# Kernel optimization log

Hardware: AMD Instinct MI355X
Metric: run time of the kernel (lower is better)

Reference implementation:

```python
import jax, jax.numpy as jnp
import numpy as np

B, T, D = 4, 2048, 1024
NF = 512
NB = 4
FREQ_SCALE = 0.1


def _w(k, shape, scale):
    return jax.random.normal(k, shape, jnp.float32) * scale


def setup_inputs() -> dict:
    key = jax.random.key(0)
    ks = jax.random.split(key, 16)
    d = D ** -0.5
    inp = {}
    inp['x'] = jax.random.normal(ks[0], (B, T, D), jnp.float32)
    inp['norm_g'] = jnp.ones((D,), jnp.float32)
    inp['norm_b'] = jnp.zeros((D,), jnp.float32)
    inp['Wconcept'] = _w(ks[1], (D, D), d); inp['bconcept'] = jnp.zeros((D,), jnp.float32)
    inp['Wcg'] = _w(ks[2], (D, D), d); inp['bcg'] = jnp.zeros((D,), jnp.float32)
    inp['Wfg'] = _w(ks[3], (NF, D), d); inp['bfg'] = jnp.zeros((NF,), jnp.float32)
    inp['Wtg'] = _w(ks[4], (1, D), d); inp['btg'] = jnp.zeros((1,), jnp.float32)
    inp['Wband'] = _w(ks[5], (NB, D), d); inp['bband'] = jnp.zeros((NB,), jnp.float32)
    inp['Wsp'] = _w(ks[6], (2 * NF, D), d)  # to_spectral, no bias
    inp['freq_importance'] = jnp.ones((NF,), jnp.float32)
    inp['log_decay'] = (jnp.linspace(-3.0, -0.001, NF) + _w(ks[7], (NF,), 0.1)).astype(jnp.float32)
    inp['frequencies'] = ((jnp.arange(NF, dtype=jnp.float32) / NF * 2.0 - 1.0) * 0.2)
    inp['dt'] = jnp.ones((NF,), jnp.float32) * 0.5
    inp['Wgate'] = _w(ks[8], (D, D), d); inp['bgate'] = jnp.zeros((D,), jnp.float32)
    inp['Wfs'] = _w(ks[9], (D, 2 * NF), (2 * NF) ** -0.5)  # from_spectral, no bias
    inp['output_scale'] = jnp.ones((1,), jnp.float32) * 0.5
    inp['norm2_g'] = jnp.ones((D,), jnp.float32)
    inp['norm2_b'] = jnp.zeros((D,), jnp.float32)
    inp['W1'] = _w(ks[10], (4 * D, D), d); inp['b1'] = jnp.zeros((4 * D,), jnp.float32)
    inp['W2'] = _w(ks[11], (D, 4 * D), (4 * D) ** -0.5); inp['b2'] = jnp.zeros((D,), jnp.float32)
    return inp


def _ln(x, g, b):
    m = jnp.mean(x, axis=-1, keepdims=True)
    v = jnp.var(x, axis=-1, keepdims=True)
    return (x - m) * jax.lax.rsqrt(v + 1e-5) * g + b


def reference(x, norm_g, norm_b, Wconcept, bconcept, Wcg, bcg, Wfg, bfg, Wtg, btg,
              Wband, bband, Wsp, freq_importance, log_decay, frequencies, dt,
              Wgate, bgate, Wfs, output_scale, norm2_g, norm2_b, W1, b1, W2, b2):
    b_, t_, _ = x.shape
    nf = log_decay.shape[0]
    nb = Wband.shape[0]
    residual = x
    xn = _ln(x, norm_g, norm_b)

    concept = xn @ Wconcept.T + bconcept
    concept_preserved = concept * jax.nn.sigmoid(xn @ Wcg.T + bcg)

    forget_gates = jax.nn.sigmoid(xn @ Wfg.T + bfg)          # (B,T,NF)
    temporal_strength = jax.nn.sigmoid(xn @ Wtg.T + btg)     # (B,T,1)
    band_strengths = jax.nn.sigmoid(xn @ Wband.T + bband)    # (B,T,NB)

    sp = xn @ Wsp.T                                          # (B,T,2*NF)
    u = jax.lax.complex(sp[..., :nf], sp[..., nf:]) * forget_gates

    decay = jax.nn.sigmoid(log_decay) * (jax.nn.softmax(freq_importance) * nf)
    omega = frequencies * FREQ_SCALE * (jax.nn.sigmoid(dt) * 2.0)
    rot = jax.lax.complex(jnp.cos(omega), jnp.sin(omega))    # (NF,)
    A = decay * rot                                          # (NF,) complex

    band_scale = jnp.repeat(band_strengths, nf // nb, axis=-1)  # (B,T,NF)
    A_exp = A * band_scale                                   # (B,T,NF) complex

    ones_first = jnp.ones((b_, 1, nf), A_exp.dtype)
    powers = jnp.cumprod(jnp.concatenate([ones_first, A_exp[:, :-1, :]], axis=1), axis=1)
    powers = powers * temporal_strength
    kernel = powers * rot

    n_fft = 2 * t_
    Uf = jnp.fft.fft(u, n=n_fft, axis=1)
    Kf = jnp.fft.fft(kernel, n=n_fft, axis=1)
    y = jnp.fft.ifft(Uf * Kf, n=n_fft, axis=1)[:, :t_, :]

    spectral_out = jnp.concatenate([y.real, y.imag], axis=-1)
    y_proj = (spectral_out @ Wfs.T) * output_scale
    gate_values = jax.nn.sigmoid(xn @ Wgate.T + bgate)
    y_gated = (y_proj * gate_values + concept_preserved) / 2.0  # dropout: eval mode

    x2 = residual + y_gated
    xn2 = _ln(x2, norm2_g, norm2_b)
    h = jax.nn.gelu(xn2 @ W1.T + b1, approximate=False)
    return x2 + h @ W2.T + b2
```

## Files before the change

### kernel.cpp

```cpp
#include <hip/hip_runtime.h>
#include <hip/hip_bf16.h>
#include <cstdint>
#include <cstddef>

typedef unsigned short u16;
typedef unsigned int u32;
typedef short bf16x8 __attribute__((ext_vector_type(8)));
typedef float f32x4 __attribute__((ext_vector_type(4)));
typedef float f32x2 __attribute__((ext_vector_type(2)));

static constexpr int Bb = 4, Tt = 2048, Dd = 1024, NFf = 512, NBb = 4;
static constexpr int Mm = Bb * Tt;
static constexpr int NZz = 4736;
static constexpr int Lc = 32;

#define DEV __device__ __forceinline__

typedef const __attribute__((address_space(1))) u32* gas_p;
typedef __attribute__((address_space(3))) u32* las_p;

DEV u16 f2bf(float f) {
    uint32_t u = __float_as_uint(f);
    u = (u + 0x7FFF + ((u >> 16) & 1)) >> 16;
    return (u16)u;
}
DEV float bf2f(u16 h) { return __uint_as_float(((uint32_t)h) << 16); }
DEV float sigm(float x) { return 1.0f / (1.0f + __expf(-x)); }
DEV float gelu_ex(float t) { return 0.5f * t * (1.0f + erff(t * 0.70710678118f)); }

DEV void xcd_swizzle(int& bx, int& by) {
    int gx = gridDim.x, nwg = gx * gridDim.y;
    int lin = blockIdx.x + gx * blockIdx.y;
    int q = nwg >> 3, r = nwg & 7;
    int xcd = lin & 7, idx = lin >> 3;
    int wg = (xcd < r) ? (xcd * (q + 1) + idx) : (r * (q + 1) + (xcd - r) * q + idx);
    bx = wg % gx; by = wg / gx;
}

static constexpr int NW0 = NZz * Dd;
static constexpr int NW1 = Dd * 2 * NFf;
static constexpr int NW2 = 4 * Dd * Dd;
static constexpr int NW3 = 4 * Dd * Dd;
static constexpr int NWTOT = NW0 + NW1 + NW2 + NW3;
static constexpr int NWB4 = NWTOT / 1024;

__global__ __launch_bounds__(256) void prep_all(
    const float* __restrict__ Wconcept, const float* __restrict__ Wcg,
    const float* __restrict__ Wfg, const float* __restrict__ Wgate,
    const float* __restrict__ Wsp, const float* __restrict__ Wtg,
    const float* __restrict__ Wband,
    const float* __restrict__ bconcept, const float* __restrict__ bcg,
    const float* __restrict__ bfg, const float* __restrict__ bgate,
    const float* __restrict__ btg, const float* __restrict__ bband,
    const float* __restrict__ Wfs, const float* __restrict__ W1,
    const float* __restrict__ W2,
    const float* __restrict__ fi, const float* __restrict__ logd,
    const float* __restrict__ freqs, const float* __restrict__ dtv,
    const float* __restrict__ x, const float* __restrict__ norm_g,
    const float* __restrict__ norm_b,
    u16* __restrict__ wcat, float* __restrict__ bias_cat,
    u16* __restrict__ wfs, u16* __restrict__ w1b, u16* __restrict__ w2b,
    float* __restrict__ rr, float* __restrict__ ri,
    float* __restrict__ Ar, float* __restrict__ Ai,
    u16* __restrict__ xn)
{
    const int bx = blockIdx.x;
    if (bx == 0) {
        __shared__ float red[256];
        int t = threadIdx.x;
        float v0 = fi[t], v1 = fi[t + 256];
        red[t] = fmaxf(v0, v1); __syncthreads();
        for (int s = 128; s; s >>= 1) { if (t < s) red[t] = fmaxf(red[t], red[t + s]); __syncthreads(); }
        float mx = red[0]; __syncthreads();
        float e0 = expf(v0 - mx), e1 = expf(v1 - mx);
        red[t] = e0 + e1; __syncthreads();
        for (int s = 128; s; s >>= 1) { if (t < s) red[t] += red[t + s]; __syncthreads(); }
        float inv = 1.0f / red[0];
#pragma unroll
        for (int k = 0; k < 2; k++) {
            int f = t + k * 256;
            float e = k ? e1 : e0;
            float decay = sigm(logd[f]) * (e * inv * (float)NFf);
            float omega = freqs[f] * 0.1f * (sigm(dtv[f]) * 2.0f);
            float cc = cosf(omega), ss = sinf(omega);
            rr[f] = cc; ri[f] = ss; Ar[f] = decay * cc; Ai[f] = decay * ss;
        }
        return;
    }
    if (bx <= NWB4) {
        const int i = ((bx - 1) * 256 + threadIdx.x) * 4;
        if (i < NW0) {
            int r = i >> 10, c = i & 1023;
            float4 v = {0.f, 0.f, 0.f, 0.f};
            if      (r < 1024) v = *(const float4*)(Wconcept + r * 1024 + c);
            else if (r < 2048) v = *(const float4*)(Wcg + (r - 1024) * 1024 + c);
            else if (r < 2560) v = *(const float4*)(Wfg + (r - 2048) * 1024 + c);
            else if (r < 3584) v = *(const float4*)(Wgate + (r - 2560) * 1024 + c);
            else if (r < 4608) v = *(const float4*)(Wsp + (r - 3584) * 1024 + c);
            else if (r == 4608) v = *(const float4*)(Wtg + c);
            else if (r < 4613) v = *(const float4*)(Wband + (r - 4609) * 1024 + c);
            ushort4 o{f2bf(v.x), f2bf(v.y), f2bf(v.z), f2bf(v.w)};
            *(ushort4*)(wcat + i) = o;
            if (c == 0) {
                float bv;
                if      (r < 1024) bv = bconcept[r];
                else if (r < 2048) bv = bcg[r - 1024];
                else if (r < 2560) bv = bfg[r - 2048];
                else if (r < 3584) bv = bgate[r - 2560];
                else if (r < 4608) bv = 0.0f;
                else if (r == 4608) bv = btg[0];
                else if (r < 4613) bv = bband[r - 4609];
                else bv = 0.0f;
                bias_cat[r] = bv;
            }
        } else if (i < NW0 + NW1) {
            int j = i - NW0;
            float4 v = *(const float4*)(Wfs + j);
            *(ushort4*)(wfs + j) = ushort4{f2bf(v.x), f2bf(v.y), f2bf(v.z), f2bf(v.w)};
        } else if (i < NW0 + NW1 + NW2) {
            int j = i - NW0 - NW1;
            float4 v = *(const float4*)(W1 + j);
            *(ushort4*)(w1b + j) = ushort4{f2bf(v.x), f2bf(v.y), f2bf(v.z), f2bf(v.w)};
        } else {
            int j = i - NW0 - NW1 - NW2;
            float4 v = *(const float4*)(W2 + j);
            *(ushort4*)(w2b + j) = ushort4{f2bf(v.x), f2bf(v.y), f2bf(v.z), f2bf(v.w)};
        }
        return;
    }
    const int m = bx - NWB4 - 1, tid = threadIdx.x;
    float4 v = ((const float4*)(x + (size_t)m * Dd))[tid];
    float s1 = v.x + v.y + v.z + v.w;
    float s2 = v.x * v.x + v.y * v.y + v.z * v.z + v.w * v.w;
    __shared__ float lds[16];
    for (int o = 32; o; o >>= 1) { s1 += __shfl_down(s1, o); s2 += __shfl_down(s2, o); }
    int lane = tid & 63, w = tid >> 6;
    if (!lane) { lds[w] = s1; lds[8 + w] = s2; }
    __syncthreads();
    s1 = lds[0] + lds[1] + lds[2] + lds[3];
    s2 = lds[8] + lds[9] + lds[10] + lds[11];
    float mean = s1 * (1.0f / Dd);
    float var  = s2 * (1.0f / Dd) - mean * mean;
    float rstd = rsqrtf(var + 1e-5f);
    float4 gv = ((const float4*)norm_g)[tid];
    float4 bv = ((const float4*)norm_b)[tid];
    ushort4 o;
    o.x = f2bf((v.x - mean) * rstd * gv.x + bv.x);
    o.y = f2bf((v.y - mean) * rstd * gv.y + bv.y);
    o.z = f2bf((v.z - mean) * rstd * gv.z + bv.z);
    o.w = f2bf((v.w - mean) * rstd * gv.w + bv.w);
    ((ushort4*)(xn + (size_t)m * Dd))[tid] = o;
}

template<int MODE>
__global__ __launch_bounds__(256, 3) void gemm_bt(
    const u16* __restrict__ A, const u16* __restrict__ Bw,
    const float* __restrict__ bias, const u16* __restrict__ addb,
    void* __restrict__ Cout, int M, int N, int K)
{
    __shared__ __align__(16) u16 smA[128 * 64];
    __shared__ __align__(16) u16 smB[128 * 64];
    const int tid = threadIdx.x;
    int bxs, bys;
    xcd_swizzle(bxs, bys);
    const int m0 = bxs * 128;
    const int n0 = bys * 128;
    const int w = tid >> 6, lane = tid & 63;
    const int wr = w >> 1, wc = w & 1;
    const int quad = lane >> 4, l16 = lane & 15;

    const int r0 = tid >> 3;
    const int cs = (tid & 7) ^ (r0 & 7);
    const u16* gA = A + (size_t)(m0 + r0) * K + cs * 8;
    const u16* gB = Bw + (size_t)(n0 + r0) * K + cs * 8;

    const int swzf = l16 & 7;

    f32x4 acc[4][4];
#pragma unroll
    for (int i = 0; i < 4; i++)
#pragma unroll
        for (int j = 0; j < 4; j++) acc[i][j] = {0.f, 0.f, 0.f, 0.f};

    for (int k0 = 0; k0 < K; k0 += 64) {
        __syncthreads();
#pragma unroll
        for (int j = 0; j < 4; j++) {
            __builtin_amdgcn_global_load_lds((gas_p)(gA + k0 + (size_t)(j * 32) * K),
                                             (las_p)(smA + j * 2048 + tid * 8), 16, 0, 0);
            __builtin_amdgcn_global_load_lds((gas_p)(gB + k0 + (size_t)(j * 32) * K),
                                             (las_p)(smB + j * 2048 + tid * 8), 16, 0, 0);
        }
        __syncthreads();
#pragma unroll
        for (int seg = 0; seg < 2; seg++) {
            bf16x8 af[4], bfv[4];
#pragma unroll
            for (int mi = 0; mi < 4; mi++)
                af[mi] = *(const bf16x8*)&smA[(wr * 64 + mi * 16 + l16) * 64 +
                                              (((seg * 4 + quad) ^ swzf) * 8)];
#pragma unroll
            for (int ni = 0; ni < 4; ni++)
                bfv[ni] = *(const bf16x8*)&smB[(wc * 64 + ni * 16 + l16) * 64 +
                                               (((seg * 4 + quad) ^ swzf) * 8)];
#pragma unroll
            for (int mi = 0; mi < 4; mi++)
#pragma unroll
                for (int ni = 0; ni < 4; ni++)
                    acc[mi][ni] = __builtin_amdgcn_mfma_f32_16x16x32_bf16(
                        af[mi], bfv[ni], acc[mi][ni], 0, 0, 0);
        }
    }

#pragma unroll
    for (int mi = 0; mi < 4; mi++) {
#pragma unroll
        for (int ni = 0; ni < 4; ni++) {
            const int gn = n0 + wc * 64 + ni * 16 + l16;
            const int gm0 = m0 + wr * 64 + mi * 16 + quad * 4;
            if constexpr (MODE == 0 || MODE == 2 || MODE == 4) {
                float bv = (MODE == 4) ? 0.0f : bias[gn];
                float t0 = acc[mi][ni][0] + bv, t1 = acc[mi][ni][1] + bv;
                float t2 = acc[mi][ni][2] + bv, t3 = acc[mi][ni][3] + bv;
                if constexpr (MODE == 2) {
                    t0 = gelu_ex(t0); t1 = gelu_ex(t1); t2 = gelu_ex(t2); t3 = gelu_ex(t3);
                }
                __hip_bfloat162 h01 = __float22bfloat162_rn(float2{t0, t1});
                __hip_bfloat162 h23 = __float22bfloat162_rn(float2{t2, t3});
                __hip_bfloat16* o = (__hip_bfloat16*)Cout;
                o[(size_t)(gm0 + 0) * N + gn] = h01.x;
                o[(size_t)(gm0 + 1) * N + gn] = h01.y;
                o[(size_t)(gm0 + 2) * N + gn] = h23.x;
                o[(size_t)(gm0 + 3) * N + gn] = h23.y;
            } else {
#pragma unroll
                for (int r = 0; r < 4; r++) {
                    const int gm = gm0 + r;
                    ((float*)Cout)[(size_t)gm * N + gn] =
                        acc[mi][ni][r] + bias[gn] + bf2f(addb[(size_t)gm * N + gn]);
                }
            }
        }
    }
}

__global__ __launch_bounds__(256) void prepAk_kernel(
    const u16* __restrict__ Z, ushort2* __restrict__ u2b,
    const float* __restrict__ Ar, const float* __restrict__ Ai,
    const float* __restrict__ rr, const float* __restrict__ ri,
    f32x2* __restrict__ k2)
{
    const int bx = blockIdx.x;
    if (bx < Mm) {
        const int m = bx, t = threadIdx.x;
        const u16* zr = Z + (size_t)m * NZz;
        ushort2 fgh = *(const ushort2*)(zr + 2048 + 2 * t);
        ushort2 spr = *(const ushort2*)(zr + 3584 + 2 * t);
        ushort2 spi = *(const ushort2*)(zr + 4096 + 2 * t);
        float fg0 = sigm(bf2f(fgh.x)), fg1 = sigm(bf2f(fgh.y));
        ushort4 o;
        o.x = f2bf(bf2f(spr.x) * fg0); o.y = f2bf(bf2f(spi.x) * fg0);
        o.z = f2bf(bf2f(spr.y) * fg1); o.w = f2bf(bf2f(spi.y) * fg1);
        ((ushort4*)u2b)[m * 256 + t] = o;
        return;
    }
    int g = (bx - Mm) * 256 + threadIdx.x;
    int b = g >> 9, f = g & (NFf - 1);
    float Pr = 1.0f, Pi = 0.0f;
    float ar = Ar[f], ai = Ai[f], cr = rr[f], ci = ri[f];
    const int band = f >> 7;
    const u16* zb = Z + (size_t)(b * Tt) * NZz;
    for (int tau = 0; tau < Lc; tau++) {
        const u16* zrow = zb + (size_t)tau * NZz;
        float tsv = sigm(bf2f(zrow[4608]));
        k2[((size_t)b * Lc + tau) * NFf + f] = f32x2{tsv * (cr * Pr - ci * Pi),
                                                     tsv * (cr * Pi + ci * Pr)};
        float bsv = sigm(bf2f(zrow[4609 + band]));
        float er = ar * bsv, ei = ai * bsv;
        float nPr = Pr * er - Pi * ei;
        float nPi = Pr * ei + Pi * er;
        Pr = nPr; Pi = nPi;
    }
}

__global__ __launch_bounds__(256) void conv_kernel(
    const ushort2* __restrict__ u2b, const f32x2* __restrict__ k2,
    u16* __restrict__ spec)
{
    __shared__ f32x2 su[96 * 64];
    __shared__ f32x2 sk[Lc * 64];
    const int tid = threadIdx.x;
    const int fl = tid & 63;
    const int ty = tid >> 6;
    const int f0 = blockIdx.x * 64;
    const int t0 = blockIdx.y * 64;
    const int b  = blockIdx.z;

    for (int i = tid; i < Lc * 64; i += 256) {
        int tau = i >> 6, ff = i & 63;
        sk[i] = k2[((size_t)b * Lc + tau) * NFf + f0 + ff];
    }
    for (int i = tid; i < 96 * 64; i += 256) {
        int r = i >> 6, ff = i & 63;
        int t = t0 - 32 + r;
        f32x2 v = {0.f, 0.f};
        if (t >= 0) {
            ushort2 h = u2b[((size_t)b * Tt + t) * NFf + f0 + ff];
            v = f32x2{bf2f(h.x), bf2f(h.y)};
        }
        su[i] = v;
    }
    __syncthreads();

    const int tl0 = 32 + ty * 16;
    f32x2 win[16], y[16];
#pragma unroll
    for (int j = 0; j < 16; j++) {
        win[j] = su[(tl0 + j) * 64 + fl];
        y[j] = f32x2{0.f, 0.f};
    }
#pragma unroll
    for (int tau = 0; tau < Lc; tau++) {
        f32x2 k = sk[tau * 64 + fl];
#pragma unroll
        for (int j = 0; j < 16; j++) {
            y[j].x += win[j].x * k.x - win[j].y * k.y;
            y[j].y += win[j].x * k.y + win[j].y * k.x;
        }
#pragma unroll
        for (int j = 15; j >= 1; j--) win[j] = win[j - 1];
        win[0] = su[(tl0 - tau - 1) * 64 + fl];
    }
#pragma unroll
    for (int j = 0; j < 16; j++) {
        size_t row = (size_t)(b * Tt + t0 + ty * 16 + j);
        spec[row * (2 * NFf) + f0 + fl]       = f2bf(y[j].x);
        spec[row * (2 * NFf) + NFf + f0 + fl] = f2bf(y[j].y);
    }
}

__global__ __launch_bounds__(256) void fuse2_ln_kernel(
    const float* __restrict__ x, const u16* __restrict__ Z,
    const u16* __restrict__ P2, const float* __restrict__ osc,
    const float* __restrict__ g2, const float* __restrict__ b2v,
    u16* __restrict__ x2b, u16* __restrict__ xn2)
{
    const int m = blockIdx.x, tid = threadIdx.x;
    const float os = osc[0];
    const u16* zr = Z + (size_t)m * NZz;
    float4 xv = ((const float4*)(x + (size_t)m * Dd))[tid];
    ushort4 pv = ((const ushort4*)(P2 + (size_t)m * Dd))[tid];
    ushort4 cv = *(const ushort4*)(zr + tid * 4);
    ushort4 gv = *(const ushort4*)(zr + 1024 + tid * 4);
    ushort4 av = *(const ushort4*)(zr + 2560 + tid * 4);
    float vals[4]; float s1 = 0.0f, s2 = 0.0f;
#pragma unroll
    for (int j = 0; j < 4; j++) {
        float concept = bf2f((&cv.x)[j]);
        float cg   = sigm(bf2f((&gv.x)[j]));
        float gate = sigm(bf2f((&av.x)[j]));
        float p = bf2f((&pv.x)[j]);
        float v = (&xv.x)[j] + 0.5f * (p * os * gate + concept * cg);
        vals[j] = v; s1 += v; s2 += v * v;
    }
    __shared__ float lds[16];
    for (int o = 32; o; o >>= 1) { s1 += __shfl_down(s1, o); s2 += __shfl_down(s2, o); }
    int lane = tid & 63, w = tid >> 6;
    if (!lane) { lds[w] = s1; lds[8 + w] = s2; }
    __syncthreads();
    s1 = lds[0] + lds[1] + lds[2] + lds[3];
    s2 = lds[8] + lds[9] + lds[10] + lds[11];
    float mean = s1 * (1.0f / Dd);
    float var  = s2 * (1.0f / Dd) - mean * mean;
    float rstd = rsqrtf(var + 1e-5f);
    ushort4 xo, no;
#pragma unroll
    for (int j = 0; j < 4; j++) {
        int d = tid * 4 + j;
        (&xo.x)[j] = f2bf(vals[j]);
        (&no.x)[j] = f2bf((vals[j] - mean) * rstd * g2[d] + b2v[d]);
    }
    ((ushort4*)(x2b + (size_t)m * Dd))[tid] = xo;
    ((ushort4*)(xn2 + (size_t)m * Dd))[tid] = no;
}

extern "C" void kernel_launch(void* const* d_in, const int* in_sizes, int n_in,
                              void* d_out, int out_size, void* d_ws, size_t ws_size,
                              hipStream_t stream)
{
    const float* x        = (const float*)d_in[0];
    const float* norm_g   = (const float*)d_in[1];
    const float* norm_b   = (const float*)d_in[2];
    const float* Wconcept = (const float*)d_in[3];
    const float* bconcept = (const float*)d_in[4];
    const float* Wcg      = (const float*)d_in[5];
    const float* bcg      = (const float*)d_in[6];
    const float* Wfg      = (const float*)d_in[7];
    const float* bfg      = (const float*)d_in[8];
    const float* Wtg      = (const float*)d_in[9];
    const float* btg      = (const float*)d_in[10];
    const float* Wband    = (const float*)d_in[11];
    const float* bband    = (const float*)d_in[12];
    const float* Wsp      = (const float*)d_in[13];
    const float* fi       = (const float*)d_in[14];
    const float* logd     = (const float*)d_in[15];
    const float* freqs    = (const float*)d_in[16];
    const float* dtv      = (const float*)d_in[17];
    const float* Wgate    = (const float*)d_in[18];
    const float* bgate    = (const float*)d_in[19];
    const float* Wfs      = (const float*)d_in[20];
    const float* osc      = (const float*)d_in[21];
    const float* n2g      = (const float*)d_in[22];
    const float* n2b      = (const float*)d_in[23];
    const float* W1       = (const float*)d_in[24];
    const float* b1       = (const float*)d_in[25];
    const float* W2       = (const float*)d_in[26];
    const float* b2       = (const float*)d_in[27];

    char* ws = (char*)d_ws;
    size_t off = 0;
    auto alloc = [&](size_t bytes) { size_t c = off; off += (bytes + 255) & ~(size_t)255; return c; };
    size_t o_wcat = alloc((size_t)NZz * Dd * 2);
    size_t o_bias = alloc((size_t)NZz * 4);
    size_t o_wfs  = alloc((size_t)Dd * 2 * NFf * 2);
    size_t o_w1   = alloc((size_t)4 * Dd * Dd * 2);
    size_t o_w2   = alloc((size_t)4 * Dd * Dd * 2);
    size_t o_xn   = alloc((size_t)Mm * Dd * 2);
    size_t o_Z    = alloc((size_t)Mm * NZz * 2);
    size_t o_u    = alloc((size_t)Mm * NFf * 4);
    size_t o_spec = alloc((size_t)Mm * Dd * 2);
    size_t o_P2   = alloc((size_t)Mm * Dd * 2);
    size_t o_k2   = alloc((size_t)Bb * Lc * NFf * 8);
    size_t o_rr   = alloc(NFf * 4);
    size_t o_ri   = alloc(NFf * 4);
    size_t o_Ar   = alloc(NFf * 4);
    size_t o_Ai   = alloc(NFf * 4);
    if (ws_size < off) return;

    u16*    wcat = (u16*)(ws + o_wcat);
    float*  bias = (float*)(ws + o_bias);
    u16*    wfs  = (u16*)(ws + o_wfs);
    u16*    w1b  = (u16*)(ws + o_w1);
    u16*    w2b  = (u16*)(ws + o_w2);
    u16*    xn   = (u16*)(ws + o_xn);
    u16*    Zb   = (u16*)(ws + o_Z);
    u16*    hb   = (u16*)(ws + o_Z);
    ushort2* u2b = (ushort2*)(ws + o_u);
    u16*    x2b  = (u16*)(ws + o_u);
    u16*    spec = (u16*)(ws + o_spec);
    u16*    xn2  = (u16*)(ws + o_spec);
    u16*    P2   = (u16*)(ws + o_P2);
    f32x2*  k2   = (f32x2*)(ws + o_k2);
    float*  rr   = (float*)(ws + o_rr);
    float*  ri   = (float*)(ws + o_ri);
    float*  Ar   = (float*)(ws + o_Ar);
    float*  Ai   = (float*)(ws + o_Ai);

    prep_all<<<1 + NWB4 + Mm, 256, 0, stream>>>(
        Wconcept, Wcg, Wfg, Wgate, Wsp, Wtg, Wband,
        bconcept, bcg, bfg, bgate, btg, bband,
        Wfs, W1, W2, fi, logd, freqs, dtv,
        x, norm_g, norm_b,
        wcat, bias, wfs, w1b, w2b, rr, ri, Ar, Ai, xn);

    gemm_bt<0><<<dim3(Mm / 128, NZz / 128), 256, 0, stream>>>(
        xn, wcat, bias, nullptr, (void*)Zb, Mm, NZz, Dd);

    prepAk_kernel<<<Mm + (Bb * NFf) / 256, 256, 0, stream>>>(
        Zb, u2b, Ar, Ai, rr, ri, k2);

    conv_kernel<<<dim3(NFf / 64, Tt / 64, Bb), 256, 0, stream>>>(u2b, k2, spec);

    gemm_bt<4><<<dim3(Mm / 128, Dd / 128), 256, 0, stream>>>(
        spec, wfs, nullptr, nullptr, (void*)P2, Mm, Dd, 2 * NFf);

    fuse2_ln_kernel<<<Mm, 256, 0, stream>>>(x, Zb, P2, osc, n2g, n2b, x2b, xn2);

    gemm_bt<2><<<dim3(Mm / 128, (4 * Dd) / 128), 256, 0, stream>>>(
        xn2, w1b, b1, nullptr, (void*)hb, Mm, 4 * Dd, Dd);
    gemm_bt<3><<<dim3(Mm / 128, Dd / 128), 256, 0, stream>>>(
        hb, w2b, b2, x2b, d_out, Mm, Dd, 4 * Dd);
}
```

Baseline: 584.1 us.

## Fuse u-computation into conv, overlap weight conversion with first GEMM, drop XCD swizzle

Moves the conversion of Wfs/W1/W2 to bf16 out of prep_all and into extra blocks of the first GEMM launch, so that work overlaps with the GEMM tail. Drops the per-row u2b buffer: conv_kernel now reads the filter gate and spectral columns straight from Z and applies the sigmoid itself, which removes one pass over memory. The trade-off is that conv now does strided u16 loads from wide Z rows instead of compact ushort2 loads. It also removes the XCD swizzle from all GEMMs in favour of plain block indexing, which may hurt L2 locality.

```diff
diff --git a/kernel.cpp b/kernel.cpp
--- a/kernel.cpp
+++ b/kernel.cpp
@@ -28,21 +28,12 @@
 DEV float sigm(float x) { return 1.0f / (1.0f + __expf(-x)); }
 DEV float gelu_ex(float t) { return 0.5f * t * (1.0f + erff(t * 0.70710678118f)); }
 
-DEV void xcd_swizzle(int& bx, int& by) {
-    int gx = gridDim.x, nwg = gx * gridDim.y;
-    int lin = blockIdx.x + gx * blockIdx.y;
-    int q = nwg >> 3, r = nwg & 7;
-    int xcd = lin & 7, idx = lin >> 3;
-    int wg = (xcd < r) ? (xcd * (q + 1) + idx) : (r * (q + 1) + (xcd - r) * q + idx);
-    bx = wg % gx; by = wg / gx;
-}
-
 static constexpr int NW0 = NZz * Dd;
 static constexpr int NW1 = Dd * 2 * NFf;
 static constexpr int NW2 = 4 * Dd * Dd;
 static constexpr int NW3 = 4 * Dd * Dd;
-static constexpr int NWTOT = NW0 + NW1 + NW2 + NW3;
-static constexpr int NWB4 = NWTOT / 1024;
+static constexpr int NWB_CAT = NW0 / 1024;
+static constexpr int NCVT = (NW1 + NW2 + NW3) / 1024;
 
 __global__ __launch_bounds__(256) void prep_all(
     const float* __restrict__ Wconcept, const float* __restrict__ Wcg,
@@ -52,14 +43,11 @@
     const float* __restrict__ bconcept, const float* __restrict__ bcg,
     const float* __restrict__ bfg, const float* __restrict__ bgate,
     const float* __restrict__ btg, const float* __restrict__ bband,
-    const float* __restrict__ Wfs, const float* __restrict__ W1,
-    const float* __restrict__ W2,
     const float* __restrict__ fi, const float* __restrict__ logd,
     const float* __restrict__ freqs, const float* __restrict__ dtv,
     const float* __restrict__ x, const float* __restrict__ norm_g,
     const float* __restrict__ norm_b,
     u16* __restrict__ wcat, float* __restrict__ bias_cat,
-    u16* __restrict__ wfs, u16* __restrict__ w1b, u16* __restrict__ w2b,
     float* __restrict__ rr, float* __restrict__ ri,
     float* __restrict__ Ar, float* __restrict__ Ai,
     u16* __restrict__ xn)
@@ -87,48 +75,33 @@
         }
         return;
     }
-    if (bx <= NWB4) {
+    if (bx <= NWB_CAT) {
         const int i = ((bx - 1) * 256 + threadIdx.x) * 4;
-        if (i < NW0) {
-            int r = i >> 10, c = i & 1023;
-            float4 v = {0.f, 0.f, 0.f, 0.f};
-            if      (r < 1024) v = *(const float4*)(Wconcept + r * 1024 + c);
-            else if (r < 2048) v = *(const float4*)(Wcg + (r - 1024) * 1024 + c);
-            else if (r < 2560) v = *(const float4*)(Wfg + (r - 2048) * 1024 + c);
-            else if (r < 3584) v = *(const float4*)(Wgate + (r - 2560) * 1024 + c);
-            else if (r < 4608) v = *(const float4*)(Wsp + (r - 3584) * 1024 + c);
-            else if (r == 4608) v = *(const float4*)(Wtg + c);
-            else if (r < 4613) v = *(const float4*)(Wband + (r - 4609) * 1024 + c);
-            ushort4 o{f2bf(v.x), f2bf(v.y), f2bf(v.z), f2bf(v.w)};
-            *(ushort4*)(wcat + i) = o;
-            if (c == 0) {
-                float bv;
-                if      (r < 1024) bv = bconcept[r];
-                else if (r < 2048) bv = bcg[r - 1024];
-                else if (r < 2560) bv = bfg[r - 2048];
-                else if (r < 3584) bv = bgate[r - 2560];
-                else if (r < 4608) bv = 0.0f;
-                else if (r == 4608) bv = btg[0];
-                else if (r < 4613) bv = bband[r - 4609];
-                else bv = 0.0f;
-                bias_cat[r] = bv;
-            }
-        } else if (i < NW0 + NW1) {
-            int j = i - NW0;
-            float4 v = *(const float4*)(Wfs + j);
-            *(ushort4*)(wfs + j) = ushort4{f2bf(v.x), f2bf(v.y), f2bf(v.z), f2bf(v.w)};
-        } else if (i < NW0 + NW1 + NW2) {
-            int j = i - NW0 - NW1;
-            float4 v = *(const float4*)(W1 + j);
-            *(ushort4*)(w1b + j) = ushort4{f2bf(v.x), f2bf(v.y), f2bf(v.z), f2bf(v.w)};
-        } else {
-            int j = i - NW0 - NW1 - NW2;
-            float4 v = *(const float4*)(W2 + j);
-            *(ushort4*)(w2b + j) = ushort4{f2bf(v.x), f2bf(v.y), f2bf(v.z), f2bf(v.w)};
+        int r = i >> 10, c = i & 1023;
+        float4 v = {0.f, 0.f, 0.f, 0.f};
+        if      (r < 1024) v = *(const float4*)(Wconcept + r * 1024 + c);
+        else if (r < 2048) v = *(const float4*)(Wcg + (r - 1024) * 1024 + c);
+        else if (r < 2560) v = *(const float4*)(Wfg + (r - 2048) * 1024 + c);
+        else if (r < 3584) v = *(const float4*)(Wgate + (r - 2560) * 1024 + c);
+        else if (r < 4608) v = *(const float4*)(Wsp + (r - 3584) * 1024 + c);
+        else if (r == 4608) v = *(const float4*)(Wtg + c);
+        else if (r < 4613) v = *(const float4*)(Wband + (r - 4609) * 1024 + c);
+        *(ushort4*)(wcat + i) = ushort4{f2bf(v.x), f2bf(v.y), f2bf(v.z), f2bf(v.w)};
+        if (c == 0) {
+            float bv;
+            if      (r < 1024) bv = bconcept[r];
+            else if (r < 2048) bv = bcg[r - 1024];
+            else if (r < 2560) bv = bfg[r - 2048];
+            else if (r < 3584) bv = bgate[r - 2560];
+            else if (r < 4608) bv = 0.0f;
+            else if (r == 4608) bv = btg[0];
+            else if (r < 4613) bv = bband[r - 4609];
+            else bv = 0.0f;
+            bias_cat[r] = bv;
         }
         return;
     }
-    const int m = bx - NWB4 - 1, tid = threadIdx.x;
+    const int m = bx - NWB_CAT - 1, tid = threadIdx.x;
     float4 v = ((const float4*)(x + (size_t)m * Dd))[tid];
     float s1 = v.x + v.y + v.z + v.w;
     float s2 = v.x * v.x + v.y * v.y + v.z * v.z + v.w * v.w;
@@ -153,18 +126,13 @@
 }
 
 template<int MODE>
-__global__ __launch_bounds__(256, 3) void gemm_bt(
-    const u16* __restrict__ A, const u16* __restrict__ Bw,
-    const float* __restrict__ bias, const u16* __restrict__ addb,
-    void* __restrict__ Cout, int M, int N, int K)
-{
-    __shared__ __align__(16) u16 smA[128 * 64];
-    __shared__ __align__(16) u16 smB[128 * 64];
+DEV void gemm_body(int m0, int n0,
+                   u16* __restrict__ smA, u16* __restrict__ smB,
+                   const u16* __restrict__ A, const u16* __restrict__ Bw,
+                   const float* __restrict__ bias, const u16* __restrict__ addb,
+                   void* __restrict__ Cout, int M, int N, int K)
+{
     const int tid = threadIdx.x;
-    int bxs, bys;
-    xcd_swizzle(bxs, bys);
-    const int m0 = bxs * 128;
-    const int n0 = bys * 128;
     const int w = tid >> 6, lane = tid & 63;
     const int wr = w >> 1, wc = w & 1;
     const int quad = lane >> 4, l16 = lane & 15;
@@ -244,27 +212,57 @@
     }
 }
 
+template<int MODE>
+__global__ __launch_bounds__(256, 3) void gemm_bt(
+    const u16* __restrict__ A, const u16* __restrict__ Bw,
+    const float* __restrict__ bias, const u16* __restrict__ addb,
+    void* __restrict__ Cout, int M, int N, int K)
+{
+    __shared__ __align__(16) u16 smA[128 * 64];
+    __shared__ __align__(16) u16 smB[128 * 64];
+    gemm_body<MODE>(blockIdx.x * 128, blockIdx.y * 128, smA, smB,
+                    A, Bw, bias, addb, Cout, M, N, K);
+}
+
+static constexpr int NG2 = (Mm / 128) * (NZz / 128);
+__global__ __launch_bounds__(256, 3) void gemm_cvt0(
+    const u16* __restrict__ A, const u16* __restrict__ Bw,
+    const float* __restrict__ bias, void* __restrict__ Cout,
+    int M, int N, int K,
+    const float* __restrict__ Wfs, const float* __restrict__ W1,
+    const float* __restrict__ W2,
+    u16* __restrict__ wfs, u16* __restrict__ w1b, u16* __restrict__ w2b)
+{
+    const int bid = blockIdx.x;
+    if (bid < NG2) {
+        __shared__ __align__(16) u16 smA[128 * 64];
+        __shared__ __align__(16) u16 smB[128 * 64];
+        gemm_body<0>((bid & 63) * 128, (bid >> 6) * 128, smA, smB,
+                     A, Bw, bias, nullptr, Cout, M, N, K);
+        return;
+    }
+    const int i = (bid - NG2) * 1024 + threadIdx.x * 4;
+    if (i < NW1) {
+        float4 v = *(const float4*)(Wfs + i);
+        *(ushort4*)(wfs + i) = ushort4{f2bf(v.x), f2bf(v.y), f2bf(v.z), f2bf(v.w)};
+    } else if (i < NW1 + NW2) {
+        int j = i - NW1;
+        float4 v = *(const float4*)(W1 + j);
+        *(ushort4*)(w1b + j) = ushort4{f2bf(v.x), f2bf(v.y), f2bf(v.z), f2bf(v.w)};
+    } else {
+        int j = i - NW1 - NW2;
+        float4 v = *(const float4*)(W2 + j);
+        *(ushort4*)(w2b + j) = ushort4{f2bf(v.x), f2bf(v.y), f2bf(v.z), f2bf(v.w)};
+    }
+}
+
 __global__ __launch_bounds__(256) void prepAk_kernel(
-    const u16* __restrict__ Z, ushort2* __restrict__ u2b,
+    const u16* __restrict__ Z,
     const float* __restrict__ Ar, const float* __restrict__ Ai,
     const float* __restrict__ rr, const float* __restrict__ ri,
     f32x2* __restrict__ k2)
 {
-    const int bx = blockIdx.x;
-    if (bx < Mm) {
-        const int m = bx, t = threadIdx.x;
-        const u16* zr = Z + (size_t)m * NZz;
-        ushort2 fgh = *(const ushort2*)(zr + 2048 + 2 * t);
-        ushort2 spr = *(const ushort2*)(zr + 3584 + 2 * t);
-        ushort2 spi = *(const ushort2*)(zr + 4096 + 2 * t);
-        float fg0 = sigm(bf2f(fgh.x)), fg1 = sigm(bf2f(fgh.y));
-        ushort4 o;
-        o.x = f2bf(bf2f(spr.x) * fg0); o.y = f2bf(bf2f(spi.x) * fg0);
-        o.z = f2bf(bf2f(spr.y) * fg1); o.w = f2bf(bf2f(spi.y) * fg1);
-        ((ushort4*)u2b)[m * 256 + t] = o;
-        return;
-    }
-    int g = (bx - Mm) * 256 + threadIdx.x;
+    int g = blockIdx.x * 256 + threadIdx.x;
     int b = g >> 9, f = g & (NFf - 1);
     float Pr = 1.0f, Pi = 0.0f;
     float ar = Ar[f], ai = Ai[f], cr = rr[f], ci = ri[f];
@@ -284,7 +282,7 @@
 }
 
 __global__ __launch_bounds__(256) void conv_kernel(
-    const ushort2* __restrict__ u2b, const f32x2* __restrict__ k2,
+    const u16* __restrict__ Z, const f32x2* __restrict__ k2,
     u16* __restrict__ spec)
 {
     __shared__ f32x2 su[96 * 64];
@@ -305,8 +303,11 @@
         int t = t0 - 32 + r;
         f32x2 v = {0.f, 0.f};
         if (t >= 0) {
-            ushort2 h = u2b[((size_t)b * Tt + t) * NFf + f0 + ff];
-            v = f32x2{bf2f(h.x), bf2f(h.y)};
+            const u16* zr = Z + (size_t)(b * Tt + t) * NZz;
+            float fg = sigm(bf2f(zr[2048 + f0 + ff]));
+            float spr = bf2f(zr[3584 + f0 + ff]);
+            float spi = bf2f(zr[4096 + f0 + ff]);
+            v = f32x2{spr * fg, spi * fg};
         }
         su[i] = v;
     }
@@ -445,7 +446,6 @@
     u16*    xn   = (u16*)(ws + o_xn);
     u16*    Zb   = (u16*)(ws + o_Z);
     u16*    hb   = (u16*)(ws + o_Z);
-    ushort2* u2b = (ushort2*)(ws + o_u);
     u16*    x2b  = (u16*)(ws + o_u);
     u16*    spec = (u16*)(ws + o_spec);
     u16*    xn2  = (u16*)(ws + o_spec);
@@ -456,20 +456,20 @@
     float*  Ar   = (float*)(ws + o_Ar);
     float*  Ai   = (float*)(ws + o_Ai);
 
-    prep_all<<<1 + NWB4 + Mm, 256, 0, stream>>>(
+    prep_all<<<1 + NWB_CAT + Mm, 256, 0, stream>>>(
         Wconcept, Wcg, Wfg, Wgate, Wsp, Wtg, Wband,
         bconcept, bcg, bfg, bgate, btg, bband,
-        Wfs, W1, W2, fi, logd, freqs, dtv,
+        fi, logd, freqs, dtv,
         x, norm_g, norm_b,
-        wcat, bias, wfs, w1b, w2b, rr, ri, Ar, Ai, xn);
-
-    gemm_bt<0><<<dim3(Mm / 128, NZz / 128), 256, 0, stream>>>(
-        xn, wcat, bias, nullptr, (void*)Zb, Mm, NZz, Dd);
-
-    prepAk_kernel<<<Mm + (Bb * NFf) / 256, 256, 0, stream>>>(
-        Zb, u2b, Ar, Ai, rr, ri, k2);
-
-    conv_kernel<<<dim3(NFf / 64, Tt / 64, Bb), 256, 0, stream>>>(u2b, k2, spec);
+        wcat, bias, rr, ri, Ar, Ai, xn);
+
+    gemm_cvt0<<<NG2 + NCVT, 256, 0, stream>>>(
+        xn, wcat, bias, (void*)Zb, Mm, NZz, Dd,
+        Wfs, W1, W2, wfs, w1b, w2b);
+
+    prepAk_kernel<<<(Bb * NFf) / 256, 256, 0, stream>>>(Zb, Ar, Ai, rr, ri, k2);
+
+    conv_kernel<<<dim3(NFf / 64, Tt / 64, Bb), 256, 0, stream>>>(Zb, k2, spec);
 
     gemm_bt<4><<<dim3(Mm / 128, Dd / 128), 256, 0, stream>>>(
         spec, wfs, nullptr, nullptr, (void*)P2, Mm, Dd, 2 * NFf);
```

New measurement: 506.5 us. 1.15x faster.
